# Performance work log

Hardware: AMD Instinct MI355X
Metric: run time of the kernel (lower is better)

Reference implementation:

```python
import jax, jax.numpy as jnp
import numpy as np

K = 20  # neighbors


def knn_idx(x, k):
    # x: [B, C, N]; returns indices of k nearest neighbors (incl. self): [B, N, k]
    xx = jnp.sum(x * x, axis=1)                          # [B, N]
    inner = jnp.einsum('bcn,bcm->bnm', x, x)             # [B, N, N]
    pd = 2.0 * inner - xx[:, :, None] - xx[:, None, :]   # -squared distance
    _, idx = jax.lax.top_k(pd, k)                        # [B, N, k]
    return idx


def graph_feature(x, k):
    # x: [B, C, N] -> edge features [B, 2C, N, k]
    idx = knn_idx(x, k)                                  # [B, N, k]
    xt = jnp.swapaxes(x, 1, 2)                           # [B, N, C]
    nbr = jax.vmap(lambda f, i: f[i])(xt, idx)           # [B, N, k, C]
    ctr = xt[:, :, None, :]                              # [B, N, 1, C]
    feat = jnp.concatenate(
        [nbr - ctr, jnp.broadcast_to(ctr, nbr.shape)], axis=-1)  # [B, N, k, 2C]
    return jnp.transpose(feat, (0, 3, 1, 2))             # [B, 2C, N, k]


def blk2(x, w, s, t):
    # 1x1 Conv2d (no bias) + folded BN + LeakyReLU(0.2); x: [B, C, N, k]
    y = jnp.einsum('oc,bcnk->bonk', w, x)
    y = y * s[None, :, None, None] + t[None, :, None, None]
    return jax.nn.leaky_relu(y, 0.2)


def blk1(x, w, s, t):
    # 1x1 Conv1d (no bias) + folded BN + LeakyReLU(0.2); x: [B, C, N]
    y = jnp.einsum('oc,bcn->bon', w, x)
    y = y * s[None, :, None] + t[None, :, None]
    return jax.nn.leaky_relu(y, 0.2)


def setup_inputs() -> dict:
    key = jax.random.key(0)
    ks = jax.random.split(key, 32)
    inp = {'x': jax.random.normal(ks[0], (16, 2, 2048), jnp.float32)}
    wdims = [(64, 4), (64, 64), (64, 128), (64, 64), (64, 128),
             (1024, 192), (512, 1216), (256, 512), (1, 256)]
    for i, (o, c) in enumerate(wdims):
        inp[f'w{i+1}'] = jax.random.normal(ks[1 + i], (o, c), jnp.float32) * np.float32((2.0 / c) ** 0.5)
    bdims = [64, 64, 64, 64, 64, 1024, 512, 256]
    for i, d in enumerate(bdims):
        inp[f's{i+1}'] = jax.random.uniform(ks[10 + i], (d,), jnp.float32, 0.5, 1.5)
        inp[f't{i+1}'] = jax.random.normal(ks[18 + i], (d,), jnp.float32) * 0.1
    return inp


def reference(x, w1, w2, w3, w4, w5, w6, w7, w8, w9,
              s1, s2, s3, s4, s5, s6, s7, s8,
              t1, t2, t3, t4, t5, t6, t7, t8):
    B, _, N = x.shape
    h = graph_feature(x, K)                 # [B, 4, N, k]
    h = blk2(h, w1, s1, t1)
    h = blk2(h, w2, s2, t2)
    x1 = jnp.max(h, axis=-1)                # [B, 64, N]
    h = graph_feature(x1, K)                # [B, 128, N, k]
    h = blk2(h, w3, s3, t3)
    h = blk2(h, w4, s4, t4)
    x2 = jnp.max(h, axis=-1)                # [B, 64, N]
    h = graph_feature(x2, K)                # [B, 128, N, k]
    h = blk2(h, w5, s5, t5)
    x3 = jnp.max(h, axis=-1)                # [B, 64, N]
    cat = jnp.concatenate([x1, x2, x3], axis=1)   # [B, 192, N]
    e = blk1(cat, w6, s6, t6)               # [B, 1024, N]
    g = jnp.max(e, axis=-1, keepdims=True)  # global max [B, 1024, 1]
    g = jnp.broadcast_to(g, (B, g.shape[1], N))
    h = jnp.concatenate([g, x1, x2, x3], axis=1)  # [B, 1216, N]
    h = blk1(h, w7, s7, t7)
    h = blk1(h, w8, s8, t8)                 # dropout = identity (eval)
    y = jnp.einsum('oc,bcn->bon', w9, h)    # [B, 1, N]
    return jax.nn.sigmoid(y.reshape(B, -1))
```

## Files before the change

kernel.cpp:

```cpp
#include <hip/hip_runtime.h>
#include <math.h>

#define KNNK 20
#define BEFORE(v1, g1, v2, g2) (((v1) > (v2)) || ((v1) == (v2) && (g1) < (g2)))

typedef unsigned short u16;
typedef unsigned int u32;
typedef unsigned long long u64;
typedef __attribute__((ext_vector_type(8))) short short8v;
typedef __attribute__((ext_vector_type(4))) float f32x4;

__device__ __forceinline__ float lrelu(float v) { return v >= 0.f ? v : 0.2f * v; }

__device__ __forceinline__ u16 f2bf(float v) {
    u32 u = __float_as_uint(v);
    u += 0x7fffu + ((u >> 16) & 1u);
    return (u16)(u >> 16);
}
__device__ __forceinline__ float bf2f(u16 h) { return __uint_as_float(((u32)h) << 16); }

__device__ __forceinline__ u32 ordf(float v) {
    u32 u = __float_as_uint(v);
    return u ^ ((u32)((int)u >> 31) | 0x80000000u);
}
__device__ __forceinline__ u64 mkkey(float v, int g) {
    return ((u64)ordf(v) << 32) | (u32)(~(u32)g);
}

__device__ __forceinline__ void cvt8(const float* __restrict__ p, short8v& H8, short8v& M8, short8v& L8) {
    float4 a = *(const float4*)(p);
    float4 b4 = *(const float4*)(p + 4);
    float v[8] = {a.x, a.y, a.z, a.w, b4.x, b4.y, b4.z, b4.w};
    short8v H, M, L;
#pragma unroll
    for (int i = 0; i < 8; ++i) {
        float x = v[i];
        u16 h = f2bf(x);
        float r1 = x - bf2f(h);
        u16 m = f2bf(r1);
        float r2 = r1 - bf2f(m);
        H[i] = (short)h;
        M[i] = (short)m;
        L[i] = (short)f2bf(r2);
    }
    H8 = H; M8 = M; L8 = L;
}

__global__ __launch_bounds__(256) void xx_kernel(const float* __restrict__ f, long bstride, int C,
                                                 float* __restrict__ xx) {
    int i = blockIdx.x * 256 + threadIdx.x;
    int b = i >> 11, n = i & 2047;
    const float* fb = f + (long)b * bstride;
    float s = 0.f;
    for (int c = 0; c < C; ++c) { float v = fb[c * 2048 + n]; s = fmaf(v, v, s); }
    xx[i] = s;
}

__device__ __forceinline__ void topk_row(const float* __restrict__ srow, int lane, int* __restrict__ orow) {
    float b1 = -INFINITY, b2 = -INFINITY, b3 = -INFINITY;
    int j1 = 0, j2 = 0, j3 = 0;
#pragma unroll
    for (int j = 0; j < 32; ++j) {
        float vv = srow[lane + 64 * j];
        bool c1 = vv > b1;
        bool c2 = vv > b2;
        bool c3 = vv > b3;
        b3 = c2 ? b2 : (c3 ? vv : b3);
        j3 = c2 ? j2 : (c3 ? j : j3);
        b2 = c1 ? b1 : (c2 ? vv : b2);
        j2 = c1 ? j1 : (c2 ? j : j2);
        b1 = c1 ? vv : b1;
        j1 = c1 ? j : j1;
    }

    u64 ka = mkkey(b1, lane + (j1 << 6));
#pragma unroll
    for (int size = 2; size <= 64; size <<= 1) {
#pragma unroll
        for (int stride = size >> 1; stride >= 1; stride >>= 1) {
            u64 ok = __shfl_xor(ka, stride);
            bool low = (lane & stride) == 0;
            bool asc = (lane & size) == 0;
            bool f = ka > ok;
            bool take = (low == asc) ? f : !f;
            ka = take ? ka : ok;
        }
    }
    u64 w19 = __shfl(ka, 19);
    unsigned used = (1u << j1) | (1u << j2) | (1u << j3);
    u64 pend = mkkey(b2, lane + (j2 << 6));
    int pstate = 0;
    while (__any(pend > w19)) {
        u64 act = __ballot(pend > w19);
        int L = __ffsll((long long)act) - 1;
        u64 ck = __shfl(pend, L);
        u64 cfb = __ballot(lane < 20 && ck > ka);
        int p = 20 - __popcll(cfb);
        u64 up = __shfl_up(ka, 1);
        if (lane < 20) {
            if (lane > p) ka = up;
            else if (lane == p) ka = ck;
        }
        if (lane == L) {
            if (pstate == 0) {
                pend = mkkey(b3, lane + (j3 << 6));
                pstate = 1;
            } else {
                float nb = -INFINITY;
                int nj = 0;
#pragma unroll
                for (int j = 0; j < 32; ++j) {
                    float vvv = ((used >> j) & 1u) ? -INFINITY : srow[lane + 64 * j];
                    if (vvv > nb) { nb = vvv; nj = j; }
                }
                used |= 1u << nj;
                pend = mkkey(nb, lane + (nj << 6));
            }
        }
        w19 = __shfl(ka, 19);
    }
    if (lane < KNNK) orow[lane] = (int)(~(u32)ka) & 2047;
}

__global__ __launch_bounds__(512, 4) void knn_kernel(const float* __restrict__ f, long bstride, int C,
                                                     const float* __restrict__ xx, int* __restrict__ idx_out) {
    __shared__ __align__(16) float pd[8 * 2048];
    __shared__ __align__(16) float Asm[16 * 64];
    int b = blockIdx.y;
    int n0 = blockIdx.x * 16;
    int t = threadIdx.x;
    const float* fb = f + (long)b * bstride;

    for (int e = t; e < C * 16; e += 512) {
        int c = e >> 4, j = e & 15;
        Asm[e] = fb[c * 2048 + n0 + j];
    }
    __syncthreads();

    float acc[16][4];
#pragma unroll
    for (int i = 0; i < 16; ++i)
#pragma unroll
        for (int j = 0; j < 4; ++j) acc[i][j] = 0.f;
    int m0 = t * 4;
    for (int c = 0; c < C; ++c) {
        float4 b4 = *(const float4*)(fb + c * 2048 + m0);
        float bv[4] = {b4.x, b4.y, b4.z, b4.w};
        const float* ar = Asm + c * 16;
        float4 a0 = *(const float4*)(ar);
        float4 a1 = *(const float4*)(ar + 4);
        float4 a2 = *(const float4*)(ar + 8);
        float4 a3 = *(const float4*)(ar + 12);
        float av[16] = {a0.x, a0.y, a0.z, a0.w, a1.x, a1.y, a1.z, a1.w,
                        a2.x, a2.y, a2.z, a2.w, a3.x, a3.y, a3.z, a3.w};
#pragma unroll
        for (int i = 0; i < 16; ++i)
#pragma unroll
            for (int j = 0; j < 4; ++j) acc[i][j] = fmaf(av[i], bv[j], acc[i][j]);
    }
    float4 xm4 = *(const float4*)(xx + b * 2048 + m0);
    float xm[4] = {xm4.x, xm4.y, xm4.z, xm4.w};

    int wave = t >> 6, lane = t & 63;

    {
        float4 xa0 = *(const float4*)(xx + b * 2048 + n0);
        float4 xa1 = *(const float4*)(xx + b * 2048 + n0 + 4);
        float xn[8] = {xa0.x, xa0.y, xa0.z, xa0.w, xa1.x, xa1.y, xa1.z, xa1.w};
#pragma unroll
        for (int i = 0; i < 8; ++i) {
            float4 o;
            o.x = (2.f * acc[i][0] - xn[i]) - xm[0];
            o.y = (2.f * acc[i][1] - xn[i]) - xm[1];
            o.z = (2.f * acc[i][2] - xn[i]) - xm[2];
            o.w = (2.f * acc[i][3] - xn[i]) - xm[3];
            *(float4*)(pd + i * 2048 + m0) = o;
        }
    }
    __syncthreads();
    topk_row(pd + wave * 2048, lane, idx_out + ((long)b * 2048 + n0 + wave) * KNNK);
    __syncthreads();

    {
        float4 xb0 = *(const float4*)(xx + b * 2048 + n0 + 8);
        float4 xb1 = *(const float4*)(xx + b * 2048 + n0 + 12);
        float xn[8] = {xb0.x, xb0.y, xb0.z, xb0.w, xb1.x, xb1.y, xb1.z, xb1.w};
#pragma unroll
        for (int i = 0; i < 8; ++i) {
            float4 o;
            o.x = (2.f * acc[8 + i][0] - xn[i]) - xm[0];
            o.y = (2.f * acc[8 + i][1] - xn[i]) - xm[1];
            o.z = (2.f * acc[8 + i][2] - xn[i]) - xm[2];
            o.w = (2.f * acc[8 + i][3] - xn[i]) - xm[3];
            *(float4*)(pd + i * 2048 + m0) = o;
        }
    }
    __syncthreads();
    topk_row(pd + wave * 2048, lane, idx_out + ((long)b * 2048 + n0 + 8 + wave) * KNNK);
}

__global__ __launch_bounds__(256) void pq_kernel(const float* __restrict__ f, long bstride, int C,
                                                 const float* __restrict__ W, float* __restrict__ P,
                                                 float* __restrict__ Q) {
    __shared__ __align__(16) float wa[64 * 64];
    __shared__ __align__(16) float wq[64 * 64];
    __shared__ __align__(16) float X[64 * 64];
    int b = blockIdx.y, n0 = blockIdx.x * 64, t = threadIdx.x;
    const float* fb = f + (long)b * bstride;
    for (int e = t; e < C * 64; e += 256) {
        int k = e >> 6, c = e & 63;
        float a = W[c * 2 * C + k];
        float bv = W[c * 2 * C + C + k];
        wa[k * 64 + c] = a;
        wq[k * 64 + c] = bv - a;
    }
    for (int e = t; e < C * 64; e += 256) {
        int k = e >> 6, j = e & 63;
        X[e] = fb[k * 2048 + n0 + j];
    }
    __syncthreads();
    int cg = t >> 4, ng = t & 15;
    float accP[4][4] = {}, accQ[4][4] = {};
    for (int k = 0; k < C; ++k) {
        float4 a4 = *(const float4*)(wa + k * 64 + cg * 4);
        float4 q4 = *(const float4*)(wq + k * 64 + cg * 4);
        float4 x4 = *(const float4*)(X + k * 64 + ng * 4);
        float av[4] = {a4.x, a4.y, a4.z, a4.w};
        float qv[4] = {q4.x, q4.y, q4.z, q4.w};
        float xv[4] = {x4.x, x4.y, x4.z, x4.w};
#pragma unroll
        for (int i = 0; i < 4; ++i)
#pragma unroll
            for (int j = 0; j < 4; ++j) {
                accP[i][j] = fmaf(av[i], xv[j], accP[i][j]);
                accQ[i][j] = fmaf(qv[i], xv[j], accQ[i][j]);
            }
    }
#pragma unroll
    for (int j = 0; j < 4; ++j) {
        long n = n0 + ng * 4 + j;
        float4 pv = {accP[0][j], accP[1][j], accP[2][j], accP[3][j]};
        float4 qv = {accQ[0][j], accQ[1][j], accQ[2][j], accQ[3][j]};
        *(float4*)(P + ((long)b * 2048 + n) * 64 + cg * 4) = pv;
        *(float4*)(Q + ((long)b * 2048 + n) * 64 + cg * 4) = qv;
    }
}

__global__ __launch_bounds__(256) void splitw3_kernel(const float* __restrict__ W, u16* __restrict__ h,
                                                      u16* __restrict__ m, u16* __restrict__ l) {
    int i = blockIdx.x * 256 + threadIdx.x;
    float v = W[i];
    u16 hh = f2bf(v);
    float r1 = v - bf2f(hh);
    u16 mm = f2bf(r1);
    float r2 = r1 - bf2f(mm);
    h[i] = hh;
    m[i] = mm;
    l[i] = f2bf(r2);
}

__global__ __launch_bounds__(256) void edge2_mfma_kernel(
    const float* __restrict__ P, const float* __restrict__ Q, const int* __restrict__ idx,
    const u16* __restrict__ Wh, const u16* __restrict__ Wm, const u16* __restrict__ Wl,
    const float* __restrict__ sa, const float* __restrict__ ta, const float* __restrict__ sb,
    const float* __restrict__ tb, float* __restrict__ out, int cofs) {
    __shared__ __align__(16) float h1t[192 * 68];
    __shared__ int idxl[160];
    int b = blockIdx.y, n0 = blockIdx.x * 8, t = threadIdx.x;
    if (t < 160) idxl[t] = idx[((long)b * 2048 + n0) * KNNK + t];
    __syncthreads();

    for (int it = t; it < 2560; it += 256) {
        int col = it % 160, cg = it / 160;
        int p = col / 20;
        int j = idxl[col];
        int n = n0 + p;
        float4 pv = *(const float4*)(P + ((long)b * 2048 + j) * 64 + cg * 4);
        float4 qv = *(const float4*)(Q + ((long)b * 2048 + n) * 64 + cg * 4);
        float4 sv = *(const float4*)(sa + cg * 4);
        float4 tv = *(const float4*)(ta + cg * 4);
        float4 o;
        o.x = lrelu(fmaf(sv.x, pv.x + qv.x, tv.x));
        o.y = lrelu(fmaf(sv.y, pv.y + qv.y, tv.y));
        o.z = lrelu(fmaf(sv.z, pv.z + qv.z, tv.z));
        o.w = lrelu(fmaf(sv.w, pv.w + qv.w, tv.w));
        *(float4*)(h1t + col * 68 + cg * 4) = o;
    }
    for (int it = t; it < 512; it += 256) {
        int col = 160 + (it & 31), cg = it >> 5;
        float4 z = {0.f, 0.f, 0.f, 0.f};
        *(float4*)(h1t + col * 68 + cg * 4) = z;
    }
    __syncthreads();

    int wave = t >> 6, lane = t & 63, l15 = lane & 15, lq = lane >> 4;
    f32x4 acc[3][4];
#pragma unroll
    for (int ct = 0; ct < 3; ++ct)
#pragma unroll
        for (int mt = 0; mt < 4; ++mt) {
            f32x4 z = {0.f, 0.f, 0.f, 0.f};
            acc[ct][mt] = z;
        }

#pragma unroll
    for (int ct = 0; ct < 3; ++ct) {
        int col = (wave * 3 + ct) * 16 + l15;
        short8v bh[2], bm[2], bl[2];
#pragma unroll
        for (int kh = 0; kh < 2; ++kh) cvt8(h1t + col * 68 + kh * 32 + lq * 8, bh[kh], bm[kh], bl[kh]);
#pragma unroll
        for (int mt = 0; mt < 4; ++mt) {
#pragma unroll
            for (int kh = 0; kh < 2; ++kh) {
                int wo = (mt * 16 + l15) * 64 + kh * 32 + lq * 8;
                short8v ah = *(const short8v*)(Wh + wo);
                short8v am = *(const short8v*)(Wm + wo);
                short8v al = *(const short8v*)(Wl + wo);
                acc[ct][mt] = __builtin_amdgcn_mfma_f32_16x16x32_bf16(ah, bh[kh], acc[ct][mt], 0, 0, 0);
                acc[ct][mt] = __builtin_amdgcn_mfma_f32_16x16x32_bf16(ah, bm[kh], acc[ct][mt], 0, 0, 0);
                acc[ct][mt] = __builtin_amdgcn_mfma_f32_16x16x32_bf16(am, bh[kh], acc[ct][mt], 0, 0, 0);
                acc[ct][mt] = __builtin_amdgcn_mfma_f32_16x16x32_bf16(am, bm[kh], acc[ct][mt], 0, 0, 0);
                acc[ct][mt] = __builtin_amdgcn_mfma_f32_16x16x32_bf16(ah, bl[kh], acc[ct][mt], 0, 0, 0);
                acc[ct][mt] = __builtin_amdgcn_mfma_f32_16x16x32_bf16(al, bh[kh], acc[ct][mt], 0, 0, 0);
            }
        }
    }
    __syncthreads();

#pragma unroll
    for (int ct = 0; ct < 3; ++ct) {
        int col = (wave * 3 + ct) * 16 + l15;
#pragma unroll
        for (int mt = 0; mt < 4; ++mt) {
            float4 d = {acc[ct][mt][0], acc[ct][mt][1], acc[ct][mt][2], acc[ct][mt][3]};
            *(float4*)(h1t + col * 68 + mt * 16 + lq * 4) = d;
        }
    }
    __syncthreads();

    for (int id = t; id < 512; id += 256) {
        int co = id & 63, p = id >> 6;
        float sv = sb[co], tv = tb[co];
        float m = -INFINITY;
#pragma unroll 4
        for (int kk = 0; kk < KNNK; ++kk)
            m = fmaxf(m, lrelu(fmaf(sv, h1t[(p * 20 + kk) * 68 + co], tv)));
        out[(long)b * (192 * 2048) + (long)(cofs + co) * 2048 + n0 + p] = m;
    }
}

__global__ __launch_bounds__(256) void edge2_kernel(
    const float* __restrict__ P, const float* __restrict__ Q, const int* __restrict__ idx,
    const float* __restrict__ W2, const float* __restrict__ sa, const float* __restrict__ ta,
    const float* __restrict__ sb, const float* __restrict__ tb, float* __restrict__ out, int cofs) {
    __shared__ __align__(16) float h1[64 * 164];
    __shared__ __align__(16) float w2l[64 * 64];
    __shared__ int idxl[160];
    int b = blockIdx.y, n0 = blockIdx.x * 8, t = threadIdx.x;
    if (t < 160) idxl[t] = idx[((long)b * 2048 + n0) * KNNK + t];
    for (int e = t; e < 4096; e += 256) { int co = e >> 6, ci = e & 63; w2l[ci * 64 + co] = W2[e]; }
    __syncthreads();
    for (int it = t; it < 2560; it += 256) {
        int col = it % 160, cg = it / 160;
        int p = col / 20;
        int j = idxl[col];
        int n = n0 + p;
        float4 pv = *(const float4*)(P + ((long)b * 2048 + j) * 64 + cg * 4);
        float4 qv = *(const float4*)(Q + ((long)b * 2048 + n) * 64 + cg * 4);
        float4 sv = *(const float4*)(sa + cg * 4);
        float4 tv = *(const float4*)(ta + cg * 4);
        h1[(cg * 4 + 0) * 164 + col] = lrelu(fmaf(sv.x, pv.x + qv.x, tv.x));
        h1[(cg * 4 + 1) * 164 + col] = lrelu(fmaf(sv.y, pv.y + qv.y, tv.y));
        h1[(cg * 4 + 2) * 164 + col] = lrelu(fmaf(sv.z, pv.z + qv.z, tv.z));
        h1[(cg * 4 + 3) * 164 + col] = lrelu(fmaf(sv.w, pv.w + qv.w, tv.w));
    }
    __syncthreads();
    int p = t & 7, co2 = t >> 3, c0 = co2 * 2;
    float acc0[20], acc1[20];
#pragma unroll
    for (int q = 0; q < 20; ++q) { acc0[q] = 0.f; acc1[q] = 0.f; }
#pragma unroll 4
    for (int k = 0; k < 64; ++k) {
        float2 w = *(const float2*)(w2l + k * 64 + c0);
        const float* hr = h1 + k * 164 + p * 20;
#pragma unroll
        for (int q = 0; q < 5; ++q) {
            float4 h4 = *(const float4*)(hr + q * 4);
            acc0[q * 4 + 0] = fmaf(w.x, h4.x, acc0[q * 4 + 0]);
            acc0[q * 4 + 1] = fmaf(w.x, h4.y, acc0[q * 4 + 1]);
            acc0[q * 4 + 2] = fmaf(w.x, h4.z, acc0[q * 4 + 2]);
            acc0[q * 4 + 3] = fmaf(w.x, h4.w, acc0[q * 4 + 3]);
            acc1[q * 4 + 0] = fmaf(w.y, h4.x, acc1[q * 4 + 0]);
            acc1[q * 4 + 1] = fmaf(w.y, h4.y, acc1[q * 4 + 1]);
            acc1[q * 4 + 2] = fmaf(w.y, h4.z, acc1[q * 4 + 2]);
            acc1[q * 4 + 3] = fmaf(w.y, h4.w, acc1[q * 4 + 3]);
        }
    }
    float s0 = sb[c0], t0v = tb[c0], s1 = sb[c0 + 1], t1v = tb[c0 + 1];
    float m0 = -INFINITY, m1 = -INFINITY;
#pragma unroll
    for (int q = 0; q < 20; ++q) {
        m0 = fmaxf(m0, lrelu(fmaf(s0, acc0[q], t0v)));
        m1 = fmaxf(m1, lrelu(fmaf(s1, acc1[q], t1v)));
    }
    out[(long)b * (192 * 2048) + (long)(cofs + c0) * 2048 + n0 + p] = m0;
    out[(long)b * (192 * 2048) + (long)(cofs + c0 + 1) * 2048 + n0 + p] = m1;
}

__global__ __launch_bounds__(256) void edge1_kernel(const float* __restrict__ P, const float* __restrict__ Q,
                                                    const int* __restrict__ idx, const float* __restrict__ s,
                                                    const float* __restrict__ tt, float* __restrict__ out,
                                                    int cofs) {
    __shared__ int idxl[80];
    int b = blockIdx.y, n0 = blockIdx.x * 4, t = threadIdx.x;
    int c = t & 63, p = t >> 6;
    if (t < 80) idxl[t] = idx[((long)b * 2048 + n0) * KNNK + t];
    __syncthreads();
    float qv = Q[((long)b * 2048 + n0 + p) * 64 + c];
    float sc = s[c], tc = tt[c];
    float m = -INFINITY;
    for (int kk = 0; kk < KNNK; ++kk) {
        int j = idxl[p * KNNK + kk];
        float v = P[((long)b * 2048 + j) * 64 + c];
        m = fmaxf(m, lrelu(fmaf(sc, v + qv, tc)));
    }
    out[(long)b * (192 * 2048) + (long)(cofs + c) * 2048 + n0 + p] = m;
}

__global__ __launch_bounds__(256) void gemm_kernel(
    const float* __restrict__ W, int ldw, int Kdim, const float* __restrict__ X, long xbstride,
    const float* __restrict__ s, const float* __restrict__ tvec, const float* __restrict__ bias, int M,
    float* __restrict__ out, long obstride, float* __restrict__ maxout) {
    __shared__ __align__(16) float wl[32 * 68];
    __shared__ __align__(16) float xl[32 * 132];
    int b = blockIdx.z, ct = blockIdx.x * 64, nt = blockIdx.y * 128, t = threadIdx.x;
    const float* Xb = X + (long)b * xbstride;
    int cg = t >> 4, ng = t & 15;
    float acc[4][8];
#pragma unroll
    for (int i = 0; i < 4; ++i)
#pragma unroll
        for (int j = 0; j < 8; ++j) acc[i][j] = 0.f;
    for (int k0 = 0; k0 < Kdim; k0 += 32) {
        __syncthreads();
        for (int e = t; e < 2048; e += 256) {
            int c = e >> 5, k = e & 31;
            wl[k * 68 + c] = W[(long)(ct + c) * ldw + k0 + k];
        }
        for (int e = t; e < 4096; e += 256) {
            int k = e >> 7, j = e & 127;
            xl[k * 132 + j] = Xb[(long)(k0 + k) * 2048 + nt + j];
        }
        __syncthreads();
#pragma unroll 8
        for (int k = 0; k < 32; ++k) {
            float4 w4 = *(const float4*)(wl + k * 68 + cg * 4);
            float4 xa = *(const float4*)(xl + k * 132 + ng * 4);
            float4 xb = *(const float4*)(xl + k * 132 + 64 + ng * 4);
            float wv[4] = {w4.x, w4.y, w4.z, w4.w};
            float xv[8] = {xa.x, xa.y, xa.z, xa.w, xb.x, xb.y, xb.z, xb.w};
#pragma unroll
            for (int i = 0; i < 4; ++i)
#pragma unroll
                for (int j = 0; j < 8; ++j) acc[i][j] = fmaf(wv[i], xv[j], acc[i][j]);
        }
    }
    if (maxout) {
        __syncthreads();
        float* scr = xl;
#pragma unroll
        for (int i = 0; i < 4; ++i) {
            int c = ct + cg * 4 + i;
            float sv = s[c], tv = tvec[c];
            float m = -INFINITY;
#pragma unroll
            for (int j = 0; j < 8; ++j) m = fmaxf(m, lrelu(fmaf(sv, acc[i][j], tv)));
            scr[(cg * 4 + i) * 16 + ng] = m;
        }
        __syncthreads();
        if (t < 64) {
            float m = scr[t * 16];
            for (int j = 1; j < 16; ++j) m = fmaxf(m, scr[t * 16 + j]);
            maxout[((long)b * M + ct + t) * 16 + blockIdx.y] = m;
        }
    } else {
#pragma unroll
        for (int i = 0; i < 4; ++i) {
            int c = ct + cg * 4 + i;
            float bv = bias ? bias[b * M + c] : 0.f;
            float sv = s[c], tv = tvec[c];
            float4 o0, o1;
            o0.x = lrelu(fmaf(sv, acc[i][0] + bv, tv));
            o0.y = lrelu(fmaf(sv, acc[i][1] + bv, tv));
            o0.z = lrelu(fmaf(sv, acc[i][2] + bv, tv));
            o0.w = lrelu(fmaf(sv, acc[i][3] + bv, tv));
            o1.x = lrelu(fmaf(sv, acc[i][4] + bv, tv));
            o1.y = lrelu(fmaf(sv, acc[i][5] + bv, tv));
            o1.z = lrelu(fmaf(sv, acc[i][6] + bv, tv));
            o1.w = lrelu(fmaf(sv, acc[i][7] + bv, tv));
            float* op = out + (long)b * obstride + (long)c * 2048 + nt + ng * 4;
            *(float4*)op = o0;
            *(float4*)(op + 64) = o1;
        }
    }
}

__global__ __launch_bounds__(256) void splitw_kernel(const float* __restrict__ W, int ldw, int koff, int K,
                                                     long total, u16* __restrict__ hi, u16* __restrict__ lo) {
    long i = (long)blockIdx.x * 256 + threadIdx.x;
    if (i >= total) return;
    long m = i / K, k = i - m * K;
    float v = W[m * ldw + koff + k];
    u16 h = f2bf(v);
    hi[i] = h;
    lo[i] = f2bf(v - bf2f(h));
}

__global__ __launch_bounds__(256) void splitx_kernel(const float* __restrict__ cat, u16* __restrict__ hi,
                                                     u16* __restrict__ lo) {
    __shared__ float lds[32][65];
    int b = blockIdx.y;
    int kt = blockIdx.x % 6, nt = blockIdx.x / 6;
    int k0 = kt * 32, n0 = nt * 64;
    int t = threadIdx.x;
#pragma unroll
    for (int i = 0; i < 8; ++i) {
        int e = t + i * 256;
        int k = e >> 6, n = e & 63;
        lds[k][n] = cat[(long)b * (192 * 2048) + (long)(k0 + k) * 2048 + n0 + n];
    }
    __syncthreads();
    int n = t >> 2, kq = t & 3;
    u16 hv[8], lv[8];
#pragma unroll
    for (int i = 0; i < 8; ++i) {
        float v = lds[kq * 8 + i][n];
        u16 h = f2bf(v);
        hv[i] = h;
        lv[i] = f2bf(v - bf2f(h));
    }
    long off = ((long)b * 2048 + n0 + n) * 192 + k0 + kq * 8;
    uint4 uh, ul;
    uh.x = (u32)hv[0] | ((u32)hv[1] << 16); uh.y = (u32)hv[2] | ((u32)hv[3] << 16);
    uh.z = (u32)hv[4] | ((u32)hv[5] << 16); uh.w = (u32)hv[6] | ((u32)hv[7] << 16);
    ul.x = (u32)lv[0] | ((u32)lv[1] << 16); ul.y = (u32)lv[2] | ((u32)lv[3] << 16);
    ul.z = (u32)lv[4] | ((u32)lv[5] << 16); ul.w = (u32)lv[6] | ((u32)lv[7] << 16);
    *(uint4*)(hi + off) = uh;
    *(uint4*)(lo + off) = ul;
}

template <int MT, int NT, bool MAXOUT>
__global__ __launch_bounds__(256, 2) void gemm_mfma(
    const u16* __restrict__ Whi, const u16* __restrict__ Wlo, const u16* __restrict__ Xhi,
    const u16* __restrict__ Xlo, int K, int M, const float* __restrict__ s,
    const float* __restrict__ tvec, const float* __restrict__ bias, float* __restrict__ outf,
    long obstride, u16* __restrict__ ohi, u16* __restrict__ olo, int oK, float* __restrict__ maxout) {
    constexpr int BM = MT * 32, BN = NT * 32;
    __shared__ __align__(16) u16 Ah[BM * 32], Al[BM * 32], Bh[BN * 32], Bl[BN * 32];
    __shared__ float scr[MAXOUT ? BM * 2 : 1];

    int b = blockIdx.z;
    int m0 = blockIdx.x * BM;
    int n0 = blockIdx.y * BN;
    int t = threadIdx.x;
    int wave = t >> 6, lane = t & 63;
    int wm = (wave >> 1) * (MT * 16);
    int wn = (wave & 1) * (NT * 16);
    const int l15 = lane & 15, lq = lane >> 4;
    const int kcs = lq ^ ((l15 >> 1) & 3);

    const u16* Xbh = Xhi + (long)b * 2048 * K;
    const u16* Xbl = Xlo + (long)b * 2048 * K;

    f32x4 zero4 = {0.f, 0.f, 0.f, 0.f};
    f32x4 acc[MT][NT];
#pragma unroll
    for (int i = 0; i < MT; ++i)
#pragma unroll
        for (int j = 0; j < NT; ++j) acc[i][j] = zero4;

    for (int k0 = 0; k0 < K; k0 += 32) {
        __syncthreads();
#pragma unroll
        for (int u = t; u < BM * 4; u += 256) {
            int row = u >> 2, kc = (u & 3) ^ ((row >> 1) & 3);
            long ga = (long)(m0 + row) * K + k0 + kc * 8;
            *(uint4*)(Ah + u * 8) = *(const uint4*)(Whi + ga);
            *(uint4*)(Al + u * 8) = *(const uint4*)(Wlo + ga);
        }
#pragma unroll
        for (int u = t; u < BN * 4; u += 256) {
            int row = u >> 2, kc = (u & 3) ^ ((row >> 1) & 3);
            long ga = (long)(n0 + row) * K + k0 + kc * 8;
            *(uint4*)(Bh + u * 8) = *(const uint4*)(Xbh + ga);
            *(uint4*)(Bl + u * 8) = *(const uint4*)(Xbl + ga);
        }
        __syncthreads();
        short8v a_h[MT], a_l[MT], b_h[NT], b_l[NT];
#pragma unroll
        for (int i = 0; i < MT; ++i) {
            int u = (wm + i * 16 + l15) * 4 + kcs;
            a_h[i] = *(const short8v*)(Ah + u * 8);
            a_l[i] = *(const short8v*)(Al + u * 8);
        }
#pragma unroll
        for (int j = 0; j < NT; ++j) {
            int u = (wn + j * 16 + l15) * 4 + kcs;
            b_h[j] = *(const short8v*)(Bh + u * 8);
            b_l[j] = *(const short8v*)(Bl + u * 8);
        }
#pragma unroll
        for (int i = 0; i < MT; ++i)
#pragma unroll
            for (int j = 0; j < NT; ++j) {
                acc[i][j] = __builtin_amdgcn_mfma_f32_16x16x32_bf16(a_h[i], b_h[j], acc[i][j], 0, 0, 0);
                acc[i][j] = __builtin_amdgcn_mfma_f32_16x16x32_bf16(a_h[i], b_l[j], acc[i][j], 0, 0, 0);
                acc[i][j] = __builtin_amdgcn_mfma_f32_16x16x32_bf16(a_l[i], b_h[j], acc[i][j], 0, 0, 0);
            }
    }

    if constexpr (MAXOUT) {
#pragma unroll
        for (int i = 0; i < MT; ++i)
#pragma unroll
            for (int r = 0; r < 4; ++r) {
                int ml = wm + i * 16 + lq * 4 + r;
                int c = m0 + ml;
                float sv = s[c], tv = tvec[c];
                float mx = -INFINITY;
#pragma unroll
                for (int j = 0; j < NT; ++j) mx = fmaxf(mx, lrelu(fmaf(sv, acc[i][j][r], tv)));
                mx = fmaxf(mx, __shfl_xor(mx, 1));
                mx = fmaxf(mx, __shfl_xor(mx, 2));
                mx = fmaxf(mx, __shfl_xor(mx, 4));
                mx = fmaxf(mx, __shfl_xor(mx, 8));
                if (l15 == 0) scr[ml * 2 + (wave & 1)] = mx;
            }
        __syncthreads();
        if (t < BM) maxout[((long)b * M + m0 + t) * 16 + blockIdx.y] = fmaxf(scr[t * 2], scr[t * 2 + 1]);
    } else if (outf) {
#pragma unroll
        for (int i = 0; i < MT; ++i)
#pragma unroll
            for (int r = 0; r < 4; ++r) {
                int c = m0 + wm + i * 16 + lq * 4 + r;
                float sv = s[c], tv = tvec[c];
                float bv = bias ? bias[b * M + c] : 0.f;
                float* op = outf + (long)b * obstride + (long)c * 2048 + n0 + wn;
#pragma unroll
                for (int j = 0; j < NT; ++j) op[j * 16 + l15] = lrelu(fmaf(sv, acc[i][j][r] + bv, tv));
            }
    } else {
#pragma unroll
        for (int i = 0; i < MT; ++i) {
            float sv[4], tv[4], bv[4];
#pragma unroll
            for (int r = 0; r < 4; ++r) {
                int c = m0 + wm + i * 16 + lq * 4 + r;
                sv[r] = s[c];
                tv[r] = tvec[c];
                bv[r] = bias ? bias[b * M + c] : 0.f;
            }
#pragma unroll
            for (int j = 0; j < NT; ++j) {
                long nb = ((long)b * 2048 + n0 + wn + j * 16 + l15) * oK + m0 + wm + i * 16 + lq * 4;
                ushort4 uh, ul;
                float v0 = lrelu(fmaf(sv[0], acc[i][j][0] + bv[0], tv[0]));
                float v1 = lrelu(fmaf(sv[1], acc[i][j][1] + bv[1], tv[1]));
                float v2 = lrelu(fmaf(sv[2], acc[i][j][2] + bv[2], tv[2]));
                float v3 = lrelu(fmaf(sv[3], acc[i][j][3] + bv[3], tv[3]));
                u16 h0 = f2bf(v0), h1 = f2bf(v1), h2 = f2bf(v2), h3 = f2bf(v3);
                uh.x = h0; uh.y = h1; uh.z = h2; uh.w = h3;
                ul.x = f2bf(v0 - bf2f(h0));
                ul.y = f2bf(v1 - bf2f(h1));
                ul.z = f2bf(v2 - bf2f(h2));
                ul.w = f2bf(v3 - bf2f(h3));
                *(ushort4*)(ohi + nb) = uh;
                *(ushort4*)(olo + nb) = ul;
            }
        }
    }
}

__global__ __launch_bounds__(256) void gmax_final(const float* __restrict__ ep, float* __restrict__ g) {
    int i = blockIdx.x * 256 + threadIdx.x;
    float m = ep[i * 16];
    for (int j = 1; j < 16; ++j) m = fmaxf(m, ep[i * 16 + j]);
    g[i] = m;
}

__global__ __launch_bounds__(64) void bias7_kernel(const float* __restrict__ w7, const float* __restrict__ g,
                                                   float* __restrict__ bias7) {
    int o = blockIdx.x;
    int b = o >> 9, co = o & 511;
    int lane = threadIdx.x;
    float acc = 0.f;
    for (int j = lane; j < 1024; j += 64) acc = fmaf(w7[(long)co * 1216 + j], g[b * 1024 + j], acc);
#pragma unroll
    for (int off = 32; off >= 1; off >>= 1) acc += __shfl_xor(acc, off);
    if (lane == 0) bias7[o] = acc;
}

__global__ __launch_bounds__(256) void w9_kernel(const float* __restrict__ w9, const float* __restrict__ h8,
                                                 float* __restrict__ out) {
    int i = blockIdx.x * 256 + threadIdx.x;
    int b = i >> 11, n = i & 2047;
    const float* hb = h8 + (long)b * 256 * 2048 + n;
    float acc = 0.f;
    for (int c = 0; c < 256; ++c) acc = fmaf(w9[c], hb[c * 2048], acc);
    out[i] = 1.f / (1.f + expf(-acc));
}

extern "C" void kernel_launch(void* const* d_in, const int* in_sizes, int n_in,
                              void* d_out, int out_size, void* d_ws, size_t ws_size,
                              hipStream_t stream) {
    (void)in_sizes; (void)n_in; (void)out_size;
    const float* x  = (const float*)d_in[0];
    const float* w1 = (const float*)d_in[1];
    const float* w2 = (const float*)d_in[2];
    const float* w3 = (const float*)d_in[3];
    const float* w4 = (const float*)d_in[4];
    const float* w5 = (const float*)d_in[5];
    const float* w6 = (const float*)d_in[6];
    const float* w7 = (const float*)d_in[7];
    const float* w8 = (const float*)d_in[8];
    const float* w9 = (const float*)d_in[9];
    const float* s1 = (const float*)d_in[10]; const float* t1 = (const float*)d_in[11];
    const float* s2 = (const float*)d_in[12]; const float* t2 = (const float*)d_in[13];
    const float* s3 = (const float*)d_in[14]; const float* t3 = (const float*)d_in[15];
    const float* s4 = (const float*)d_in[16]; const float* t4 = (const float*)d_in[17];
    const float* s5 = (const float*)d_in[18]; const float* t5 = (const float*)d_in[19];
    const float* s6 = (const float*)d_in[20]; const float* t6 = (const float*)d_in[21];
    const float* s7 = (const float*)d_in[22]; const float* t7 = (const float*)d_in[23];
    const float* s8 = (const float*)d_in[24]; const float* t8 = (const float*)d_in[25];

    float* cat = (float*)d_ws;
    float* xxb = cat + (long)6291456;
    int* idxb = (int*)(xxb + 32768);
    float* ep = (float*)(idxb + 655360);
    float* g  = ep + 262144;
    float* b7 = g + 16384;
    float* h8 = b7 + 8192;
    float* P  = h8 + 8388608;
    float* Q  = P + 2097152;
    u16* h7hi = (u16*)(Q + 2097152);
    u16* h7lo = h7hi + 16777216;
    u16* cathi = h7lo + 16777216;
    u16* catlo = cathi + 6291456;
    u16* w6h = catlo + 6291456;
    u16* w6l = w6h + 196608;
    u16* w7h = w6l + 196608;
    u16* w7l = w7h + 98304;
    u16* w8h = w7l + 98304;
    u16* w8l = w8h + 131072;
    const size_t NEED = 173375488;
    bool big = ws_size >= NEED;

    u16* w2L = h7hi;
    u16* w4L = h7hi + 12288;

    dim3 blk(256);
    dim3 blk512(512);
    long catstride = 192 * 2048;

    if (big) {
        splitw3_kernel<<<16, blk, 0, stream>>>(w2, w2L, w2L + 4096, w2L + 8192);
        splitw3_kernel<<<16, blk, 0, stream>>>(w4, w4L, w4L + 4096, w4L + 8192);
    }

    xx_kernel<<<128, blk, 0, stream>>>(x, 2 * 2048, 2, xxb);
    knn_kernel<<<dim3(128, 16), blk512, 0, stream>>>(x, 2 * 2048, 2, xxb, idxb);
    pq_kernel<<<dim3(32, 16), blk, 0, stream>>>(x, 2 * 2048, 2, w1, P, Q);
    if (big)
        edge2_mfma_kernel<<<dim3(256, 16), blk, 0, stream>>>(P, Q, idxb, w2L, w2L + 4096, w2L + 8192,
                                                             s1, t1, s2, t2, cat, 0);
    else
        edge2_kernel<<<dim3(256, 16), blk, 0, stream>>>(P, Q, idxb, w2, s1, t1, s2, t2, cat, 0);
    xx_kernel<<<128, blk, 0, stream>>>(cat, catstride, 64, xxb);
    knn_kernel<<<dim3(128, 16), blk512, 0, stream>>>(cat, catstride, 64, xxb, idxb);
    pq_kernel<<<dim3(32, 16), blk, 0, stream>>>(cat, catstride, 64, w3, P, Q);
    if (big)
        edge2_mfma_kernel<<<dim3(256, 16), blk, 0, stream>>>(P, Q, idxb, w4L, w4L + 4096, w4L + 8192,
                                                             s3, t3, s4, t4, cat, 64);
    else
        edge2_kernel<<<dim3(256, 16), blk, 0, stream>>>(P, Q, idxb, w4, s3, t3, s4, t4, cat, 64);
    xx_kernel<<<128, blk, 0, stream>>>(cat + 64 * 2048, catstride, 64, xxb);
    knn_kernel<<<dim3(128, 16), blk512, 0, stream>>>(cat + 64 * 2048, catstride, 64, xxb, idxb);
    pq_kernel<<<dim3(32, 16), blk, 0, stream>>>(cat + 64 * 2048, catstride, 64, w5, P, Q);
    edge1_kernel<<<dim3(512, 16), blk, 0, stream>>>(P, Q, idxb, s5, t5, cat, 128);

    if (big) {
        splitw_kernel<<<768, blk, 0, stream>>>(w6, 192, 0, 192, 196608, w6h, w6l);
        splitw_kernel<<<384, blk, 0, stream>>>(w7, 1216, 1024, 192, 98304, w7h, w7l);
        splitw_kernel<<<512, blk, 0, stream>>>(w8, 512, 0, 512, 131072, w8h, w8l);
        splitx_kernel<<<dim3(192, 16), blk, 0, stream>>>(cat, cathi, catlo);
        gemm_mfma<4, 4, true><<<dim3(8, 16, 16), blk, 0, stream>>>(
            w6h, w6l, cathi, catlo, 192, 1024, s6, t6, nullptr, nullptr, 0, nullptr, nullptr, 0, ep);
        gmax_final<<<64, blk, 0, stream>>>(ep, g);
        bias7_kernel<<<dim3(16 * 512), dim3(64), 0, stream>>>(w7, g, b7);
        gemm_mfma<4, 4, false><<<dim3(4, 16, 16), blk, 0, stream>>>(
            w7h, w7l, cathi, catlo, 192, 512, s7, t7, b7, nullptr, 0, h7hi, h7lo, 512, nullptr);
        gemm_mfma<2, 4, false><<<dim3(4, 16, 16), blk, 0, stream>>>(
            w8h, w8l, h7hi, h7lo, 512, 256, s8, t8, nullptr, h8, (long)256 * 2048, nullptr, nullptr, 0,
            nullptr);
        w9_kernel<<<128, blk, 0, stream>>>(w9, h8, (float*)d_out);
    } else {
        float* h7f = (float*)h7hi;
        gemm_kernel<<<dim3(16, 16, 16), blk, 0, stream>>>(w6, 192, 192, cat, catstride, s6, t6, nullptr,
                                                          1024, nullptr, 0, ep);
        gmax_final<<<64, blk, 0, stream>>>(ep, g);
        bias7_kernel<<<dim3(16 * 512), dim3(64), 0, stream>>>(w7, g, b7);
        gemm_kernel<<<dim3(8, 16, 16), blk, 0, stream>>>(w7 + 1024, 1216, 192, cat, catstride, s7, t7, b7,
                                                         512, h7f, (long)512 * 2048, nullptr);
        gemm_kernel<<<dim3(4, 16, 16), blk, 0, stream>>>(w8, 512, 512, h7f, (long)512 * 2048, s8, t8,
                                                         nullptr, 256, h8, (long)256 * 2048, nullptr);
        w9_kernel<<<128, blk, 0, stream>>>(w9, h8, (float*)d_out);
    }
}
```

Before: 1.010 ms.

## Use bf16x3 MFMA for 64-channel kNN distance with split-half top-k merge

For the two 64-channel kNN stages, a new kernel first splits features into transposed hi/mid/lo bf16 parts. A second kernel computes the pairwise inner products with MFMA instructions using a 6-product bf16x3 emulation of fp32. Top-k now runs on two 1024-column halves held in a smaller LDS buffer, and the two partial top-20 lists are merged with a bitonic sort. This moves the N^2 distance FLOPs off scalar FMA onto matrix cores, at the cost of an extra split pass, extra global traffic, and possible rounding differences that can flip near-tied neighbour choices.

```diff
diff --git a/kernel.cpp b/kernel.cpp
--- a/kernel.cpp
+++ b/kernel.cpp
@@ -72,7 +72,6 @@
         b1 = c1 ? vv : b1;
         j1 = c1 ? j : j1;
     }
-
     u64 ka = mkkey(b1, lane + (j1 << 6));
 #pragma unroll
     for (int size = 2; size <= 64; size <<= 1) {
@@ -122,6 +121,89 @@
     if (lane < KNNK) orow[lane] = (int)(~(u32)ka) & 2047;
 }
 
+__device__ __forceinline__ u64 topk20_half(const float* __restrict__ srow, int lane, int colbase) {
+    float b1 = -INFINITY, b2 = -INFINITY, b3 = -INFINITY;
+    int j1 = 0, j2 = 0, j3 = 0;
+#pragma unroll
+    for (int j = 0; j < 16; ++j) {
+        float vv = srow[lane + 64 * j];
+        bool c1 = vv > b1;
+        bool c2 = vv > b2;
+        bool c3 = vv > b3;
+        b3 = c2 ? b2 : (c3 ? vv : b3);
+        j3 = c2 ? j2 : (c3 ? j : j3);
+        b2 = c1 ? b1 : (c2 ? vv : b2);
+        j2 = c1 ? j1 : (c2 ? j : j2);
+        b1 = c1 ? vv : b1;
+        j1 = c1 ? j : j1;
+    }
+    u64 ka = mkkey(b1, colbase + lane + (j1 << 6));
+#pragma unroll
+    for (int size = 2; size <= 64; size <<= 1) {
+#pragma unroll
+        for (int stride = size >> 1; stride >= 1; stride >>= 1) {
+            u64 ok = __shfl_xor(ka, stride);
+            bool low = (lane & stride) == 0;
+            bool asc = (lane & size) == 0;
+            bool f = ka > ok;
+            bool take = (low == asc) ? f : !f;
+            ka = take ? ka : ok;
+        }
+    }
+    u64 w19 = __shfl(ka, 19);
+    unsigned used = (1u << j1) | (1u << j2) | (1u << j3);
+    u64 pend = mkkey(b2, colbase + lane + (j2 << 6));
+    int pstate = 0;
+    while (__any(pend > w19)) {
+        u64 act = __ballot(pend > w19);
+        int L = __ffsll((long long)act) - 1;
+        u64 ck = __shfl(pend, L);
+        u64 cfb = __ballot(lane < 20 && ck > ka);
+        int p = 20 - __popcll(cfb);
+        u64 up = __shfl_up(ka, 1);
+        if (lane < 20) {
+            if (lane > p) ka = up;
+            else if (lane == p) ka = ck;
+        }
+        if (lane == L) {
+            if (pstate == 0) {
+                pend = mkkey(b3, colbase + lane + (j3 << 6));
+                pstate = 1;
+            } else {
+                float nb = -INFINITY;
+                int nj = 0;
+#pragma unroll
+                for (int j = 0; j < 16; ++j) {
+                    float vvv = ((used >> j) & 1u) ? -INFINITY : srow[lane + 64 * j];
+                    if (vvv > nb) { nb = vvv; nj = j; }
+                }
+                used |= 1u << nj;
+                pend = mkkey(nb, colbase + lane + (nj << 6));
+            }
+        }
+        w19 = __shfl(ka, 19);
+    }
+    return ka;
+}
+
+__device__ __forceinline__ u64 merge20(u64 kA, u64 kB, int lane) {
+    u64 kb = __shfl(kB, (lane - 20) & 63);
+    u64 ka = lane < 20 ? kA : (lane < 40 ? kb : 0ULL);
+#pragma unroll
+    for (int size = 2; size <= 64; size <<= 1) {
+#pragma unroll
+        for (int stride = size >> 1; stride >= 1; stride >>= 1) {
+            u64 ok = __shfl_xor(ka, stride);
+            bool low = (lane & stride) == 0;
+            bool asc = (lane & size) == 0;
+            bool f = ka > ok;
+            bool take = (low == asc) ? f : !f;
+            ka = take ? ka : ok;
+        }
+    }
+    return ka;
+}
+
 __global__ __launch_bounds__(512, 4) void knn_kernel(const float* __restrict__ f, long bstride, int C,
                                                      const float* __restrict__ xx, int* __restrict__ idx_out) {
     __shared__ __align__(16) float pd[8 * 2048];
@@ -197,6 +279,121 @@
     }
     __syncthreads();
     topk_row(pd + wave * 2048, lane, idx_out + ((long)b * 2048 + n0 + 8 + wave) * KNNK);
+}
+
+__global__ __launch_bounds__(256) void split3t_kernel(const float* __restrict__ src, long bstride,
+                                                      u16* __restrict__ oh, u16* __restrict__ om,
+                                                      u16* __restrict__ ol) {
+    __shared__ float lds[32][65];
+    int b = blockIdx.y;
+    int kt = blockIdx.x & 1, nt = blockIdx.x >> 1;
+    int k0 = kt * 32, n0 = nt * 64, t = threadIdx.x;
+#pragma unroll
+    for (int i = 0; i < 8; ++i) {
+        int e = t + i * 256;
+        int k = e >> 6, n = e & 63;
+        lds[k][n] = src[(long)b * bstride + (long)(k0 + k) * 2048 + n0 + n];
+    }
+    __syncthreads();
+    int n = t >> 2, kq = t & 3;
+    u16 hv[8], mv[8], lv[8];
+#pragma unroll
+    for (int i = 0; i < 8; ++i) {
+        float v = lds[kq * 8 + i][n];
+        u16 h = f2bf(v);
+        float r1 = v - bf2f(h);
+        u16 m = f2bf(r1);
+        float r2 = r1 - bf2f(m);
+        hv[i] = h; mv[i] = m; lv[i] = f2bf(r2);
+    }
+    long off = ((long)b * 2048 + n0 + n) * 64 + k0 + kq * 8;
+    uint4 uh, um, ul;
+    uh.x = (u32)hv[0] | ((u32)hv[1] << 16); uh.y = (u32)hv[2] | ((u32)hv[3] << 16);
+    uh.z = (u32)hv[4] | ((u32)hv[5] << 16); uh.w = (u32)hv[6] | ((u32)hv[7] << 16);
+    um.x = (u32)mv[0] | ((u32)mv[1] << 16); um.y = (u32)mv[2] | ((u32)mv[3] << 16);
+    um.z = (u32)mv[4] | ((u32)mv[5] << 16); um.w = (u32)mv[6] | ((u32)mv[7] << 16);
+    ul.x = (u32)lv[0] | ((u32)lv[1] << 16); ul.y = (u32)lv[2] | ((u32)lv[3] << 16);
+    ul.z = (u32)lv[4] | ((u32)lv[5] << 16); ul.w = (u32)lv[6] | ((u32)lv[7] << 16);
+    *(uint4*)(oh + off) = uh;
+    *(uint4*)(om + off) = um;
+    *(uint4*)(ol + off) = ul;
+}
+
+__global__ __launch_bounds__(512, 4) void knn_mfma_kernel(const u16* __restrict__ Sh, const u16* __restrict__ Sm,
+                                                          const u16* __restrict__ Sl, const float* __restrict__ xx,
+                                                          int* __restrict__ idx_out) {
+    __shared__ __align__(16) float pd[16 * 1028];
+    int b = blockIdx.y, n0 = blockIdx.x * 16, t = threadIdx.x;
+    int wave = t >> 6, lane = t & 63, l15 = lane & 15, lq = lane >> 4;
+    const u16* bh_ = Sh + (long)b * 2048 * 64;
+    const u16* bm_ = Sm + (long)b * 2048 * 64;
+    const u16* bl_ = Sl + (long)b * 2048 * 64;
+
+    long ab = (long)(n0 + l15) * 64 + lq * 8;
+    short8v ah0 = *(const short8v*)(bh_ + ab), ah1 = *(const short8v*)(bh_ + ab + 32);
+    short8v am0 = *(const short8v*)(bm_ + ab), am1 = *(const short8v*)(bm_ + ab + 32);
+    short8v al0 = *(const short8v*)(bl_ + ab), al1 = *(const short8v*)(bl_ + ab + 32);
+    float4 xn4 = *(const float4*)(xx + b * 2048 + n0 + lq * 4);
+    float xn[4] = {xn4.x, xn4.y, xn4.z, xn4.w};
+
+    u64 kA0 = 0, kA1 = 0, kB0 = 0, kB1 = 0;
+#pragma unroll
+    for (int half = 0; half < 2; ++half) {
+        int jb = half * 1024 + wave * 128;
+        short8v Bh0[2], Bh1[2], Bm0[2], Bm1[2], Bl0[2], Bl1[2];
+        {
+            long bb = (long)(jb + l15) * 64 + lq * 8;
+            Bh0[0] = *(const short8v*)(bh_ + bb); Bh1[0] = *(const short8v*)(bh_ + bb + 32);
+            Bm0[0] = *(const short8v*)(bm_ + bb); Bm1[0] = *(const short8v*)(bm_ + bb + 32);
+            Bl0[0] = *(const short8v*)(bl_ + bb); Bl1[0] = *(const short8v*)(bl_ + bb + 32);
+        }
+#pragma unroll
+        for (int tt = 0; tt < 8; ++tt) {
+            const int cur = tt & 1, nxt = cur ^ 1;
+            if (tt < 7) {
+                long bb = (long)(jb + (tt + 1) * 16 + l15) * 64 + lq * 8;
+                Bh0[nxt] = *(const short8v*)(bh_ + bb); Bh1[nxt] = *(const short8v*)(bh_ + bb + 32);
+                Bm0[nxt] = *(const short8v*)(bm_ + bb); Bm1[nxt] = *(const short8v*)(bm_ + bb + 32);
+                Bl0[nxt] = *(const short8v*)(bl_ + bb); Bl1[nxt] = *(const short8v*)(bl_ + bb + 32);
+            }
+            f32x4 p = {0.f, 0.f, 0.f, 0.f}, q = {0.f, 0.f, 0.f, 0.f};
+            p = __builtin_amdgcn_mfma_f32_16x16x32_bf16(ah0, Bh0[cur], p, 0, 0, 0);
+            q = __builtin_amdgcn_mfma_f32_16x16x32_bf16(ah0, Bm0[cur], q, 0, 0, 0);
+            p = __builtin_amdgcn_mfma_f32_16x16x32_bf16(am0, Bh0[cur], p, 0, 0, 0);
+            q = __builtin_amdgcn_mfma_f32_16x16x32_bf16(am0, Bm0[cur], q, 0, 0, 0);
+            p = __builtin_amdgcn_mfma_f32_16x16x32_bf16(ah0, Bl0[cur], p, 0, 0, 0);
+            q = __builtin_amdgcn_mfma_f32_16x16x32_bf16(al0, Bh0[cur], q, 0, 0, 0);
+            p = __builtin_amdgcn_mfma_f32_16x16x32_bf16(ah1, Bh1[cur], p, 0, 0, 0);
+            q = __builtin_amdgcn_mfma_f32_16x16x32_bf16(ah1, Bm1[cur], q, 0, 0, 0);
+            p = __builtin_amdgcn_mfma_f32_16x16x32_bf16(am1, Bh1[cur], p, 0, 0, 0);
+            q = __builtin_amdgcn_mfma_f32_16x16x32_bf16(am1, Bm1[cur], q, 0, 0, 0);
+            p = __builtin_amdgcn_mfma_f32_16x16x32_bf16(ah1, Bl1[cur], p, 0, 0, 0);
+            q = __builtin_amdgcn_mfma_f32_16x16x32_bf16(al1, Bh1[cur], q, 0, 0, 0);
+            int col = jb + tt * 16 + l15;
+            float xmc = xx[(long)b * 2048 + col];
+            f32x4 r = p + q;
+            int lcol = col - half * 1024;
+            pd[(lq * 4 + 0) * 1028 + lcol] = (2.f * r[0] - xn[0]) - xmc;
+            pd[(lq * 4 + 1) * 1028 + lcol] = (2.f * r[1] - xn[1]) - xmc;
+            pd[(lq * 4 + 2) * 1028 + lcol] = (2.f * r[2] - xn[2]) - xmc;
+            pd[(lq * 4 + 3) * 1028 + lcol] = (2.f * r[3] - xn[3]) - xmc;
+        }
+        __syncthreads();
+        if (half == 0) {
+            kA0 = topk20_half(pd + (2 * wave) * 1028, lane, 0);
+            kA1 = topk20_half(pd + (2 * wave + 1) * 1028, lane, 0);
+            __syncthreads();
+        } else {
+            kB0 = topk20_half(pd + (2 * wave) * 1028, lane, 1024);
+            kB1 = topk20_half(pd + (2 * wave + 1) * 1028, lane, 1024);
+        }
+    }
+    u64 f0 = merge20(kA0, kB0, lane);
+    u64 f1 = merge20(kA1, kB1, lane);
+    if (lane < KNNK) {
+        idx_out[((long)b * 2048 + n0 + 2 * wave) * KNNK + lane] = (int)(~(u32)f0) & 2047;
+        idx_out[((long)b * 2048 + n0 + 2 * wave + 1) * KNNK + lane] = (int)(~(u32)f1) & 2047;
+    }
 }
 
 __global__ __launch_bounds__(256) void pq_kernel(const float* __restrict__ f, long bstride, int C,
@@ -759,6 +956,9 @@
 
     u16* w2L = h7hi;
     u16* w4L = h7hi + 12288;
+    u16* Sh = h7hi + 32768;
+    u16* Sm = Sh + 2097152;
+    u16* Sl = Sm + 2097152;
 
     dim3 blk(256);
     dim3 blk512(512);
@@ -778,7 +978,12 @@
     else
         edge2_kernel<<<dim3(256, 16), blk, 0, stream>>>(P, Q, idxb, w2, s1, t1, s2, t2, cat, 0);
     xx_kernel<<<128, blk, 0, stream>>>(cat, catstride, 64, xxb);
-    knn_kernel<<<dim3(128, 16), blk512, 0, stream>>>(cat, catstride, 64, xxb, idxb);
+    if (big) {
+        split3t_kernel<<<dim3(64, 16), blk, 0, stream>>>(cat, catstride, Sh, Sm, Sl);
+        knn_mfma_kernel<<<dim3(128, 16), blk512, 0, stream>>>(Sh, Sm, Sl, xxb, idxb);
+    } else {
+        knn_kernel<<<dim3(128, 16), blk512, 0, stream>>>(cat, catstride, 64, xxb, idxb);
+    }
     pq_kernel<<<dim3(32, 16), blk, 0, stream>>>(cat, catstride, 64, w3, P, Q);
     if (big)
         edge2_mfma_kernel<<<dim3(256, 16), blk, 0, stream>>>(P, Q, idxb, w4L, w4L + 4096, w4L + 8192,
@@ -786,7 +991,12 @@
     else
         edge2_kernel<<<dim3(256, 16), blk, 0, stream>>>(P, Q, idxb, w4, s3, t3, s4, t4, cat, 64);
     xx_kernel<<<128, blk, 0, stream>>>(cat + 64 * 2048, catstride, 64, xxb);
-    knn_kernel<<<dim3(128, 16), blk512, 0, stream>>>(cat + 64 * 2048, catstride, 64, xxb, idxb);
+    if (big) {
+        split3t_kernel<<<dim3(64, 16), blk, 0, stream>>>(cat + 64 * 2048, catstride, Sh, Sm, Sl);
+        knn_mfma_kernel<<<dim3(128, 16), blk512, 0, stream>>>(Sh, Sm, Sl, xxb, idxb);
+    } else {
+        knn_kernel<<<dim3(128, 16), blk512, 0, stream>>>(cat + 64 * 2048, catstride, 64, xxb, idxb);
+    }
     pq_kernel<<<dim3(32, 16), blk, 0, stream>>>(cat + 64 * 2048, catstride, 64, w5, P, Q);
     edge1_kernel<<<dim3(512, 16), blk, 0, stream>>>(P, Q, idxb, s5, t5, cat, 128);
 
```

Result: slower. 1.192 ms (+17.9%).
